# Kernel tuning notes

Measured on AMD Instinct MI355X. Metric: run time of the kernel, lower is better.

The kernel has to match this reference:

```python
import jax, jax.numpy as jnp
import numpy as np
import math

D_MODEL = 1024
D_K = 1024
D_V = 1024
B, S = 4, 2048


def setup_inputs() -> dict:
    key = jax.random.key(0)
    ks = jax.random.split(key, 6)
    scale = 1.0 / math.sqrt(D_MODEL)
    return {
        "q": jax.random.normal(ks[0], (B, S, D_MODEL), dtype=jnp.float32),
        "k": jax.random.normal(ks[1], (B, S, D_MODEL), dtype=jnp.float32),
        "v": jax.random.normal(ks[2], (B, S, D_MODEL), dtype=jnp.float32),
        "Wq": jax.random.normal(ks[3], (D_K, D_MODEL), dtype=jnp.float32) * scale,
        "bq": jnp.zeros((D_K,), dtype=jnp.float32),
        "Wk": jax.random.normal(ks[4], (D_K, D_MODEL), dtype=jnp.float32) * scale,
        "bk": jnp.zeros((D_K,), dtype=jnp.float32),
        "Wv": jax.random.normal(ks[5], (D_V, D_MODEL), dtype=jnp.float32) * scale,
        "bv": jnp.zeros((D_V,), dtype=jnp.float32),
    }


def reference(q, k, v, Wq, bq, Wk, bk, Wv, bv):
    # Linear projections (torch Linear: x @ W.T + b)
    qp = jnp.einsum("bsd,kd->bsk", q, Wq) + bq   # [B,S,d_k]
    kp = jnp.einsum("bsd,kd->bsk", k, Wk) + bk   # [B,S,d_k]
    vp = jnp.einsum("bsd,kd->bsk", v, Wv) + bv   # [B,S,d_v]
    # Scaled dot-product attention, full NxN score matrix as in source
    energies = jnp.einsum("bqk,bsk->bqs", qp, kp) / math.sqrt(D_K)  # [B,S,S]
    weights = jax.nn.softmax(energies, axis=-1)
    out = jnp.einsum("bqs,bsv->bqv", weights, vp)  # [B,S,d_v]
    return out
```

## Files before the change

### kernel.cpp

```cpp
#include <hip/hip_runtime.h>
#include <hip/hip_bf16.h>


typedef __attribute__((ext_vector_type(8))) short short8;
typedef __attribute__((ext_vector_type(4))) float f32x4;

static __device__ __forceinline__ int swz(int b) {
    return b ^ (((b >> 6) & 7) << 4);
}

static __device__ __forceinline__ unsigned short f2bf(float f) {
    unsigned u = __float_as_uint(f);
    u += 0x7FFFu + ((u >> 16) & 1u);
    return (unsigned short)(u >> 16);
}

static __device__ __forceinline__ float bf2f(unsigned short s) {
    return __uint_as_float(((unsigned)s) << 16);
}

template <typename T>
static __device__ __forceinline__ void load16bf(const T* __restrict__ g, short8& lo, short8& hi) {
    if constexpr (sizeof(T) == 4) {
        const f32x4* p = reinterpret_cast<const f32x4*>(g);
        f32x4 a = p[0], b = p[1], c = p[2], d = p[3];
#pragma unroll
        for (int j = 0; j < 4; ++j) lo[j]     = (short)f2bf(a[j]);
#pragma unroll
        for (int j = 0; j < 4; ++j) lo[4 + j] = (short)f2bf(b[j]);
#pragma unroll
        for (int j = 0; j < 4; ++j) hi[j]     = (short)f2bf(c[j]);
#pragma unroll
        for (int j = 0; j < 4; ++j) hi[4 + j] = (short)f2bf(d[j]);
    } else {
        const short8* p = reinterpret_cast<const short8*>(g);
        lo = p[0];
        hi = p[1];
    }
}

template <typename TA, typename TB, bool OUT_BF16, bool HAS_BIAS>
__global__ __launch_bounds__(256) void gemm_bt(
    const TA* __restrict__ A, const TB* __restrict__ B,
    const float* __restrict__ bias, void* __restrict__ Cv,
    int M, int N, int K, long sA, long sB, long sC, float scale)
{
    __shared__ __align__(16) char lds[2][2][128 * 64];
    const int tid = threadIdx.x;
    const long bz = blockIdx.z;
    A += bz * sA;
    B += bz * sB;
    const int row0 = blockIdx.y * 128, col0 = blockIdx.x * 128;

    const int r = tid >> 1, h = tid & 1;
    const TA* ga = A + (long)(row0 + r) * K + h * 16;
    const TB* gb = B + (long)(col0 + r) * K + h * 16;
    const int w0 = swz(r * 64 + h * 32);
    const int w1 = swz(r * 64 + h * 32 + 16);

    const int lane = tid & 63, wid = tid >> 6;
    const int wr = wid >> 1, wc = wid & 1;
    const int fq = lane >> 4, fr = lane & 15;

    int ra[4], rb[4];
#pragma unroll
    for (int i = 0; i < 4; ++i) {
        ra[i] = swz((wr * 64 + i * 16 + fr) * 64 + fq * 16);
        rb[i] = swz((wc * 64 + i * 16 + fr) * 64 + fq * 16);
    }

    f32x4 acc[4][4] = {};

    const int KT = K >> 5;
    short8 la0, la1, lb0, lb1;
    load16bf(ga, la0, la1);
    load16bf(gb, lb0, lb1);
    *(short8*)(&lds[0][0][0] + w0) = la0;
    *(short8*)(&lds[0][0][0] + w1) = la1;
    *(short8*)(&lds[0][1][0] + w0) = lb0;
    *(short8*)(&lds[0][1][0] + w1) = lb1;
    __syncthreads();

    for (int kt = 0; kt < KT; ++kt) {
        const int cur = kt & 1;
        const bool more = (kt + 1 < KT);
        if (more) {
            load16bf(ga + (kt + 1) * 32, la0, la1);
            load16bf(gb + (kt + 1) * 32, lb0, lb1);
        }
        char* pa = &lds[cur][0][0];
        char* pb = &lds[cur][1][0];
        short8 af[4], bfg[4];
#pragma unroll
        for (int i = 0; i < 4; ++i) af[i] = *(const short8*)(pa + ra[i]);
#pragma unroll
        for (int i = 0; i < 4; ++i) bfg[i] = *(const short8*)(pb + rb[i]);
#pragma unroll
        for (int mi = 0; mi < 4; ++mi)
#pragma unroll
            for (int ni = 0; ni < 4; ++ni)
                acc[mi][ni] = __builtin_amdgcn_mfma_f32_16x16x32_bf16(
                    af[mi], bfg[ni], acc[mi][ni], 0, 0, 0);
        if (more) {
            char* qa = &lds[cur ^ 1][0][0];
            char* qb = &lds[cur ^ 1][1][0];
            *(short8*)(qa + w0) = la0;
            *(short8*)(qa + w1) = la1;
            *(short8*)(qb + w0) = lb0;
            *(short8*)(qb + w1) = lb1;
        }
        __syncthreads();
    }

    float bcol[4];
#pragma unroll
    for (int ni = 0; ni < 4; ++ni)
        bcol[ni] = HAS_BIAS ? bias[col0 + wc * 64 + ni * 16 + fr] : 0.f;

#pragma unroll
    for (int mi = 0; mi < 4; ++mi) {
#pragma unroll
        for (int ni = 0; ni < 4; ++ni) {
            const int cc = col0 + wc * 64 + ni * 16 + fr;
#pragma unroll
            for (int j = 0; j < 4; ++j) {
                const int rr = row0 + wr * 64 + mi * 16 + fq * 4 + j;
                const float vv = acc[mi][ni][j] * scale + bcol[ni];
                if constexpr (OUT_BF16) {
                    ((unsigned short*)Cv)[bz * sC + (long)rr * N + cc] = f2bf(vv);
                } else {
                    ((float*)Cv)[bz * sC + (long)rr * N + cc] = vv;
                }
            }
        }
    }
}

__global__ __launch_bounds__(256) void softmax_rows(unsigned short* __restrict__ P, int S) {
    const long row = blockIdx.x;
    unsigned short* p = P + row * (long)S;
    const int tid = threadIdx.x;
    const int wid = tid >> 6, lane = tid & 63;

    short8 v = *(const short8*)(p + tid * 8);
    float x[8];
#pragma unroll
    for (int j = 0; j < 8; ++j) x[j] = bf2f((unsigned short)v[j]);

    float m = x[0];
#pragma unroll
    for (int j = 1; j < 8; ++j) m = fmaxf(m, x[j]);
#pragma unroll
    for (int off = 32; off > 0; off >>= 1) m = fmaxf(m, __shfl_xor(m, off));
    __shared__ float red[8];
    if (lane == 0) red[wid] = m;
    __syncthreads();
    m = fmaxf(fmaxf(red[0], red[1]), fmaxf(red[2], red[3]));

    float e[8], s = 0.f;
#pragma unroll
    for (int j = 0; j < 8; ++j) { e[j] = __expf(x[j] - m); s += e[j]; }
#pragma unroll
    for (int off = 32; off > 0; off >>= 1) s += __shfl_xor(s, off);
    if (lane == 0) red[4 + wid] = s;
    __syncthreads();
    s = red[4] + red[5] + red[6] + red[7];
    const float inv = 1.f / s;

    short8 o;
#pragma unroll
    for (int j = 0; j < 8; ++j) o[j] = (short)f2bf(e[j] * inv);
    *(short8*)(p + tid * 8) = o;
}

__global__ __launch_bounds__(256) void transpose_bf16(
    const unsigned short* __restrict__ in, unsigned short* __restrict__ out, int R, int C)
{
    __shared__ unsigned short t[64][72];
    const long z = blockIdx.z;
    in  += z * (long)R * C;
    out += z * (long)R * C;
    const int r0 = blockIdx.y * 64, c0 = blockIdx.x * 64;
    const int tid = threadIdx.x;

    const int r = tid >> 2, cc = (tid & 3) * 16;
    const short8* src = (const short8*)(in + (long)(r0 + r) * C + c0 + cc);
    short8 v0 = src[0], v1 = src[1];
#pragma unroll
    for (int j = 0; j < 8; ++j) {
        t[r][cc + j]     = (unsigned short)v0[j];
        t[r][cc + 8 + j] = (unsigned short)v1[j];
    }
    __syncthreads();

    const int c = tid >> 2, rr = (tid & 3) * 16;
    short8 o0, o1;
#pragma unroll
    for (int j = 0; j < 8; ++j) {
        o0[j] = (short)t[rr + j][c];
        o1[j] = (short)t[rr + 8 + j][c];
    }
    short8* dst = (short8*)(out + (long)(c0 + c) * R + r0 + rr);
    dst[0] = o0;
    dst[1] = o1;
}

extern "C" void kernel_launch(void* const* d_in, const int* in_sizes, int n_in,
                              void* d_out, int out_size, void* d_ws, size_t ws_size,
                              hipStream_t stream) {
    const float* q  = (const float*)d_in[0];
    const float* k  = (const float*)d_in[1];
    const float* v  = (const float*)d_in[2];
    const float* Wq = (const float*)d_in[3];
    const float* bq = (const float*)d_in[4];
    const float* Wk = (const float*)d_in[5];
    const float* bk = (const float*)d_in[6];
    const float* Wv = (const float*)d_in[7];
    const float* bv = (const float*)d_in[8];

    const int S = 2048, D = 1024;
    const long MB = 1024L * 1024L;
    char* ws = (char*)d_ws;
    unsigned short* qp  = (unsigned short*)(ws + 0 * MB);
    unsigned short* kp  = (unsigned short*)(ws + 16 * MB);
    unsigned short* vp  = (unsigned short*)(ws + 32 * MB);
    unsigned short* vpT = (unsigned short*)(ws + 48 * MB);
    unsigned short* P   = (unsigned short*)(ws + 64 * MB);

    dim3 blk(256);

    gemm_bt<float, float, true, true><<<dim3(8, 64, 1), blk, 0, stream>>>(
        q, Wq, bq, qp, 8192, 1024, 1024, 0, 0, 0, 1.f);
    gemm_bt<float, float, true, true><<<dim3(8, 64, 1), blk, 0, stream>>>(
        k, Wk, bk, kp, 8192, 1024, 1024, 0, 0, 0, 1.f);
    gemm_bt<float, float, true, true><<<dim3(8, 64, 1), blk, 0, stream>>>(
        v, Wv, bv, vp, 8192, 1024, 1024, 0, 0, 0, 1.f);

    gemm_bt<unsigned short, unsigned short, true, false><<<dim3(16, 16, 4), blk, 0, stream>>>(
        qp, kp, nullptr, P, 2048, 2048, 1024,
        (long)S * D, (long)S * D, (long)S * S, 0.03125f);

    softmax_rows<<<dim3(4 * S), blk, 0, stream>>>(P, S);

    transpose_bf16<<<dim3(16, 32, 4), blk, 0, stream>>>(vp, vpT, S, D);

    gemm_bt<unsigned short, unsigned short, false, false><<<dim3(8, 16, 4), blk, 0, stream>>>(
        P, vpT, nullptr, (float*)d_out, 2048, 1024, 2048,
        (long)S * S, (long)D * S, (long)S * D, 1.f);
}
```

Before: 413.9 us.

## Pre-convert inputs to bf16 and load GEMM tiles via direct global-to-LDS

New measurement: 390.5 us. 5.6% less time.

```diff
diff --git a/kernel.cpp b/kernel.cpp
--- a/kernel.cpp
+++ b/kernel.cpp
@@ -2,113 +2,98 @@
 #include <hip/hip_bf16.h>
 
 
+typedef unsigned short u16;
 typedef __attribute__((ext_vector_type(8))) short short8;
 typedef __attribute__((ext_vector_type(4))) float f32x4;
 
-static __device__ __forceinline__ int swz(int b) {
-    return b ^ (((b >> 6) & 7) << 4);
-}
-
-static __device__ __forceinline__ unsigned short f2bf(float f) {
+typedef const __attribute__((address_space(1))) void* gptr_t;
+typedef __attribute__((address_space(3))) void* sptr_t;
+
+static __device__ __forceinline__ u16 f2bf(float f) {
     unsigned u = __float_as_uint(f);
     u += 0x7FFFu + ((u >> 16) & 1u);
-    return (unsigned short)(u >> 16);
-}
-
-static __device__ __forceinline__ float bf2f(unsigned short s) {
+    return (u16)(u >> 16);
+}
+static __device__ __forceinline__ float bf2f(u16 s) {
     return __uint_as_float(((unsigned)s) << 16);
 }
 
-template <typename T>
-static __device__ __forceinline__ void load16bf(const T* __restrict__ g, short8& lo, short8& hi) {
-    if constexpr (sizeof(T) == 4) {
-        const f32x4* p = reinterpret_cast<const f32x4*>(g);
-        f32x4 a = p[0], b = p[1], c = p[2], d = p[3];
-#pragma unroll
-        for (int j = 0; j < 4; ++j) lo[j]     = (short)f2bf(a[j]);
-#pragma unroll
-        for (int j = 0; j < 4; ++j) lo[4 + j] = (short)f2bf(b[j]);
-#pragma unroll
-        for (int j = 0; j < 4; ++j) hi[j]     = (short)f2bf(c[j]);
-#pragma unroll
-        for (int j = 0; j < 4; ++j) hi[4 + j] = (short)f2bf(d[j]);
-    } else {
-        const short8* p = reinterpret_cast<const short8*>(g);
-        lo = p[0];
-        hi = p[1];
-    }
-}
-
-template <typename TA, typename TB, bool OUT_BF16, bool HAS_BIAS>
+static __device__ __forceinline__ void gll16(const u16* g, u16* l) {
+    __builtin_amdgcn_global_load_lds((gptr_t)g, (sptr_t)l, 16, 0, 0);
+}
+
+__global__ __launch_bounds__(256) void cvt2(
+    const float* __restrict__ a, u16* __restrict__ oa, long na,
+    const float* __restrict__ b, u16* __restrict__ ob, long nb)
+{
+    const float* s = blockIdx.z ? b : a;
+    u16* d = blockIdx.z ? ob : oa;
+    const long n = blockIdx.z ? nb : na;
+    const long stride = (long)gridDim.x * blockDim.x * 8;
+    for (long i = ((long)blockIdx.x * blockDim.x + threadIdx.x) * 8; i < n; i += stride) {
+        f32x4 x = *(const f32x4*)(s + i);
+        f32x4 y = *(const f32x4*)(s + i + 4);
+        short8 o;
+#pragma unroll
+        for (int j = 0; j < 4; ++j) { o[j] = (short)f2bf(x[j]); o[4 + j] = (short)f2bf(y[j]); }
+        *(short8*)(d + i) = o;
+    }
+}
+
+template <bool OUT_BF16, bool HAS_BIAS>
 __global__ __launch_bounds__(256) void gemm_bt(
-    const TA* __restrict__ A, const TB* __restrict__ B,
+    const u16* __restrict__ A, const u16* __restrict__ B,
     const float* __restrict__ bias, void* __restrict__ Cv,
     int M, int N, int K, long sA, long sB, long sC, float scale)
 {
-    __shared__ __align__(16) char lds[2][2][128 * 64];
+    __shared__ __align__(16) u16 lA[4096], lB[4096];
     const int tid = threadIdx.x;
     const long bz = blockIdx.z;
     A += bz * sA;
     B += bz * sB;
     const int row0 = blockIdx.y * 128, col0 = blockIdx.x * 128;
-
-    const int r = tid >> 1, h = tid & 1;
-    const TA* ga = A + (long)(row0 + r) * K + h * 16;
-    const TB* gb = B + (long)(col0 + r) * K + h * 16;
-    const int w0 = swz(r * 64 + h * 32);
-    const int w1 = swz(r * 64 + h * 32 + 16);
-
     const int lane = tid & 63, wid = tid >> 6;
+
+    const int srow = wid * 16 + (lane >> 2);
+    const int scol = (lane & 3) * 8;
+    const u16* ga = A + (long)(row0 + srow) * K + scol;
+    const u16* gb = B + (long)(col0 + srow) * K + scol;
+    const long g1 = 64L * K;
+    u16* la0 = lA + wid * 512;
+    u16* la1 = lA + 2048 + wid * 512;
+    u16* lb0 = lB + wid * 512;
+    u16* lb1 = lB + 2048 + wid * 512;
+
     const int wr = wid >> 1, wc = wid & 1;
     const int fq = lane >> 4, fr = lane & 15;
-
-    int ra[4], rb[4];
+    const u16* pa[4];
+    const u16* pb[4];
 #pragma unroll
     for (int i = 0; i < 4; ++i) {
-        ra[i] = swz((wr * 64 + i * 16 + fr) * 64 + fq * 16);
-        rb[i] = swz((wc * 64 + i * 16 + fr) * 64 + fq * 16);
+        pa[i] = lA + (wr * 64 + i * 16 + fr) * 32 + fq * 8;
+        pb[i] = lB + (wc * 64 + i * 16 + fr) * 32 + fq * 8;
     }
 
     f32x4 acc[4][4] = {};
-
     const int KT = K >> 5;
-    short8 la0, la1, lb0, lb1;
-    load16bf(ga, la0, la1);
-    load16bf(gb, lb0, lb1);
-    *(short8*)(&lds[0][0][0] + w0) = la0;
-    *(short8*)(&lds[0][0][0] + w1) = la1;
-    *(short8*)(&lds[0][1][0] + w0) = lb0;
-    *(short8*)(&lds[0][1][0] + w1) = lb1;
-    __syncthreads();
-
     for (int kt = 0; kt < KT; ++kt) {
-        const int cur = kt & 1;
-        const bool more = (kt + 1 < KT);
-        if (more) {
-            load16bf(ga + (kt + 1) * 32, la0, la1);
-            load16bf(gb + (kt + 1) * 32, lb0, lb1);
-        }
-        char* pa = &lds[cur][0][0];
-        char* pb = &lds[cur][1][0];
-        short8 af[4], bfg[4];
-#pragma unroll
-        for (int i = 0; i < 4; ++i) af[i] = *(const short8*)(pa + ra[i]);
-#pragma unroll
-        for (int i = 0; i < 4; ++i) bfg[i] = *(const short8*)(pb + rb[i]);
+        const long ko = (long)kt * 32;
+        gll16(ga + ko, la0);
+        gll16(ga + ko + g1, la1);
+        gll16(gb + ko, lb0);
+        gll16(gb + ko + g1, lb1);
+        __syncthreads();
+        short8 af[4], bf[4];
+#pragma unroll
+        for (int i = 0; i < 4; ++i) af[i] = *(const short8*)pa[i];
+#pragma unroll
+        for (int i = 0; i < 4; ++i) bf[i] = *(const short8*)pb[i];
 #pragma unroll
         for (int mi = 0; mi < 4; ++mi)
 #pragma unroll
             for (int ni = 0; ni < 4; ++ni)
                 acc[mi][ni] = __builtin_amdgcn_mfma_f32_16x16x32_bf16(
-                    af[mi], bfg[ni], acc[mi][ni], 0, 0, 0);
-        if (more) {
-            char* qa = &lds[cur ^ 1][0][0];
-            char* qb = &lds[cur ^ 1][1][0];
-            *(short8*)(qa + w0) = la0;
-            *(short8*)(qa + w1) = la1;
-            *(short8*)(qb + w0) = lb0;
-            *(short8*)(qb + w1) = lb1;
-        }
+                    af[mi], bf[ni], acc[mi][ni], 0, 0, 0);
         __syncthreads();
     }
 
@@ -127,7 +112,7 @@
                 const int rr = row0 + wr * 64 + mi * 16 + fq * 4 + j;
                 const float vv = acc[mi][ni][j] * scale + bcol[ni];
                 if constexpr (OUT_BF16) {
-                    ((unsigned short*)Cv)[bz * sC + (long)rr * N + cc] = f2bf(vv);
+                    ((u16*)Cv)[bz * sC + (long)rr * N + cc] = f2bf(vv);
                 } else {
                     ((float*)Cv)[bz * sC + (long)rr * N + cc] = vv;
                 }
@@ -136,16 +121,16 @@
     }
 }
 
-__global__ __launch_bounds__(256) void softmax_rows(unsigned short* __restrict__ P, int S) {
+__global__ __launch_bounds__(256) void softmax_rows(u16* __restrict__ P, int S) {
     const long row = blockIdx.x;
-    unsigned short* p = P + row * (long)S;
+    u16* p = P + row * (long)S;
     const int tid = threadIdx.x;
     const int wid = tid >> 6, lane = tid & 63;
 
     short8 v = *(const short8*)(p + tid * 8);
     float x[8];
 #pragma unroll
-    for (int j = 0; j < 8; ++j) x[j] = bf2f((unsigned short)v[j]);
+    for (int j = 0; j < 8; ++j) x[j] = bf2f((u16)v[j]);
 
     float m = x[0];
 #pragma unroll
@@ -174,9 +159,9 @@
 }
 
 __global__ __launch_bounds__(256) void transpose_bf16(
-    const unsigned short* __restrict__ in, unsigned short* __restrict__ out, int R, int C)
+    const u16* __restrict__ in, u16* __restrict__ out, int R, int C)
 {
-    __shared__ unsigned short t[64][72];
+    __shared__ u16 t[64][72];
     const long z = blockIdx.z;
     in  += z * (long)R * C;
     out += z * (long)R * C;
@@ -188,8 +173,8 @@
     short8 v0 = src[0], v1 = src[1];
 #pragma unroll
     for (int j = 0; j < 8; ++j) {
-        t[r][cc + j]     = (unsigned short)v0[j];
-        t[r][cc + 8 + j] = (unsigned short)v1[j];
+        t[r][cc + j]     = (u16)v0[j];
+        t[r][cc + 8 + j] = (u16)v1[j];
     }
     __syncthreads();
 
@@ -219,32 +204,38 @@
     const float* bv = (const float*)d_in[8];
 
     const int S = 2048, D = 1024;
-    const long MB = 1024L * 1024L;
+    const long MiB = 1024L * 1024L;
+    const long nQ = 4L * S * D;
+    const long nW = (long)D * D;
     char* ws = (char*)d_ws;
-    unsigned short* qp  = (unsigned short*)(ws + 0 * MB);
-    unsigned short* kp  = (unsigned short*)(ws + 16 * MB);
-    unsigned short* vp  = (unsigned short*)(ws + 32 * MB);
-    unsigned short* vpT = (unsigned short*)(ws + 48 * MB);
-    unsigned short* P   = (unsigned short*)(ws + 64 * MB);
+    u16* sb  = (u16*)(ws + 0 * MiB);
+    u16* wb  = (u16*)(ws + 16 * MiB);
+    u16* qp  = (u16*)(ws + 18 * MiB);
+    u16* kp  = (u16*)(ws + 34 * MiB);
+    u16* vp  = (u16*)(ws + 50 * MiB);
+    u16* P   = (u16*)(ws + 66 * MiB);
+    u16* vpT = (u16*)(ws + 0 * MiB);
 
     dim3 blk(256);
-
-    gemm_bt<float, float, true, true><<<dim3(8, 64, 1), blk, 0, stream>>>(
-        q, Wq, bq, qp, 8192, 1024, 1024, 0, 0, 0, 1.f);
-    gemm_bt<float, float, true, true><<<dim3(8, 64, 1), blk, 0, stream>>>(
-        k, Wk, bk, kp, 8192, 1024, 1024, 0, 0, 0, 1.f);
-    gemm_bt<float, float, true, true><<<dim3(8, 64, 1), blk, 0, stream>>>(
-        v, Wv, bv, vp, 8192, 1024, 1024, 0, 0, 0, 1.f);
-
-    gemm_bt<unsigned short, unsigned short, true, false><<<dim3(16, 16, 4), blk, 0, stream>>>(
-        qp, kp, nullptr, P, 2048, 2048, 1024,
-        (long)S * D, (long)S * D, (long)S * S, 0.03125f);
+    dim3 gproj(8, 64, 1);
+
+    cvt2<<<dim3(512, 1, 2), blk, 0, stream>>>(q, sb, nQ, Wq, wb, nW);
+    gemm_bt<true, true><<<gproj, blk, 0, stream>>>(sb, wb, bq, qp,
+        8192, 1024, 1024, 0, 0, 0, 1.f);
+    cvt2<<<dim3(512, 1, 2), blk, 0, stream>>>(k, sb, nQ, Wk, wb, nW);
+    gemm_bt<true, true><<<gproj, blk, 0, stream>>>(sb, wb, bk, kp,
+        8192, 1024, 1024, 0, 0, 0, 1.f);
+    cvt2<<<dim3(512, 1, 2), blk, 0, stream>>>(v, sb, nQ, Wv, wb, nW);
+    gemm_bt<true, true><<<gproj, blk, 0, stream>>>(sb, wb, bv, vp,
+        8192, 1024, 1024, 0, 0, 0, 1.f);
+
+    transpose_bf16<<<dim3(16, 32, 4), blk, 0, stream>>>(vp, vpT, S, D);
+
+    gemm_bt<true, false><<<dim3(16, 16, 4), blk, 0, stream>>>(qp, kp, nullptr, P,
+        2048, 2048, 1024, (long)S * D, (long)S * D, (long)S * S, 0.03125f);
 
     softmax_rows<<<dim3(4 * S), blk, 0, stream>>>(P, S);
 
-    transpose_bf16<<<dim3(16, 32, 4), blk, 0, stream>>>(vp, vpT, S, D);
-
-    gemm_bt<unsigned short, unsigned short, false, false><<<dim3(8, 16, 4), blk, 0, stream>>>(
-        P, vpT, nullptr, (float*)d_out, 2048, 1024, 2048,
-        (long)S * S, (long)D * S, (long)S * D, 1.f);
-}
+    gemm_bt<false, false><<<dim3(8, 16, 4), blk, 0, stream>>>(P, vpT, nullptr,
+        (float*)d_out, 2048, 1024, 2048, (long)S * S, (long)D * S, (long)S * D, 1.f);
+}
```
